# Optimization experiments

Measured on AMD Instinct MI355X. Metric: run time of the kernel, lower is better.

The kernel has to match this reference:

```python
import jax, jax.numpy as jnp
import numpy as np

NEG = 9000000000000000.0  # large negative multiplier from the original code

def setup_inputs() -> dict:
    key = jax.random.key(0)
    ks = jax.random.split(key, 7)
    B, N, DIN, H, DOUT = 128, 512, 256, 256, 256
    x = jax.random.normal(ks[0], (B, N, DIN), dtype=jnp.float32)
    # binary float mask (1 = attend, 0 = blocked), as used multiplicatively in the module
    mask = (jax.random.uniform(ks[1], (B, N, N)) > 0.5).astype(jnp.float32)
    def lin(k, fan_in, fan_out):
        kw, kb = jax.random.split(k)
        bound = 1.0 / np.sqrt(fan_in)
        W = jax.random.uniform(kw, (fan_in, fan_out), minval=-bound, maxval=bound, dtype=jnp.float32)
        b = jax.random.uniform(kb, (fan_out,), minval=-bound, maxval=bound, dtype=jnp.float32)
        return W, b
    Wv, bv = lin(ks[2], DIN, H)
    Wk, bk = lin(ks[3], DIN, H)
    Wq, bq = lin(ks[4], DIN, H)
    Wo, bo = lin(ks[5], H, DOUT)
    return {"x": x, "mask": mask, "Wv": Wv, "bv": bv, "Wk": Wk, "bk": bk,
            "Wq": Wq, "bq": bq, "Wo": Wo, "bo": bo}

def reference(x, mask, Wv, bv, Wk, bk, Wq, bq, Wo, bo):
    # x: [B,N,din], mask: [B,N,N]
    v = jax.nn.relu(jnp.einsum('bnd,dh->bnh', x, Wv) + bv)   # [B,N,H]
    q = jax.nn.relu(jnp.einsum('bnd,dh->bnh', x, Wq) + bq)   # [B,N,H]
    k = jax.nn.relu(jnp.einsum('bnd,dh->bnh', x, Wk) + bk)   # [B,N,H]
    scores = jnp.einsum('bnh,bmh->bnm', q, k)                 # [B,N,N]
    att = jax.nn.softmax(scores * mask - NEG * (1.0 - mask), axis=2)
    out = jnp.einsum('bnm,bmh->bnh', att, v)                  # [B,N,H]
    out = jax.nn.relu(jnp.einsum('bnh,ho->bno', out, Wo) + bo)
    return out
```

## Files before the change

kernel.cpp:

```cpp
#include <hip/hip_runtime.h>
#include <stdint.h>

typedef __attribute__((ext_vector_type(8))) __bf16 bf16x8;
typedef __attribute__((ext_vector_type(4))) float f32x4;
typedef __attribute__((ext_vector_type(8))) unsigned short ushort8;
typedef __attribute__((ext_vector_type(4))) unsigned short ushort4v;
typedef unsigned short u16;
typedef unsigned int u32;

__device__ __forceinline__ u16 f2bf(float f) {
    __bf16 h = (__bf16)f;
    return __builtin_bit_cast(u16, h);
}

__device__ __forceinline__ f32x4 mfma16(bf16x8 a, bf16x8 b, f32x4 c) {
    return __builtin_amdgcn_mfma_f32_16x16x32_bf16(a, b, c, 0, 0, 0);
}

typedef __attribute__((address_space(1))) const char g_char;
typedef __attribute__((address_space(3))) char l_char;
__device__ __forceinline__ void gload_lds16(const void* g, void* l) {
    __builtin_amdgcn_global_load_lds((g_char*)g, (l_char*)l, 16, 0, 0);
}

__global__ __launch_bounds__(256) void prep_w(
    const float* __restrict__ Wq, const float* __restrict__ Wk,
    const float* __restrict__ Wv, const float* __restrict__ Wo,
    u16* __restrict__ WT, u16* __restrict__ WOT)
{
    int idx = blockIdx.x * 256 + threadIdx.x;
    if (idx < 196608) {
        int j = idx >> 8, k = idx & 255;
        const float* W = (j < 256) ? Wq : (j < 512) ? Wk : Wv;
        WT[idx] = f2bf(W[k * 256 + (j & 255)]);
    } else {
        int t = idx - 196608;
        int j = t >> 8, k = t & 255;
        WOT[t] = f2bf(Wo[k * 256 + j]);
    }
}

__global__ __launch_bounds__(256, 2) void qkv_gemm(
    const float* __restrict__ X, const u16* __restrict__ WT,
    const float* __restrict__ bQ, const float* __restrict__ bK,
    const float* __restrict__ bV,
    u16* __restrict__ outQ, u16* __restrict__ outK, u16* __restrict__ outVT)
{
    __shared__ __align__(16) u16 As[128 * 256];
    __shared__ __align__(16) u16 Bs[128 * 64];
    const int tid = threadIdx.x;
    const int m0 = blockIdx.x * 128;

    #pragma unroll
    for (int i = 0; i < 32; ++i) {
        int flat = (i * 256 + tid) * 4;
        int r = flat >> 8, c = flat & 255;
        const f32x4 f = *reinterpret_cast<const f32x4*>(X + (size_t)(m0 + r) * 256 + c);
        ushort4v h;
        h.x = f2bf(f.x); h.y = f2bf(f.y); h.z = f2bf(f.z); h.w = f2bf(f.w);
        int byte = (r * 512 + c * 2) ^ ((r & 7) << 4);
        *reinterpret_cast<ushort4v*>(reinterpret_cast<char*>(As) + byte) = h;
    }

    const int lane = tid & 63, wid = tid >> 6;
    const int wr = wid >> 1, wc = wid & 1;
    const int lr = lane & 15, lg = lane >> 4;

    for (int cb = 0; cb < 6; ++cb) {
        const int jbase = cb * 128;
        f32x4 acc[4][4];
        #pragma unroll
        for (int a = 0; a < 4; ++a)
            #pragma unroll
            for (int b = 0; b < 4; ++b) acc[a][b] = (f32x4){0.f, 0.f, 0.f, 0.f};

        for (int kk = 0; kk < 256; kk += 64) {
            __syncthreads();
            #pragma unroll
            for (int i = 0; i < 4; ++i) {
                int e = (i * 256 + tid) * 8;
                int r = e >> 6, c = e & 63;
                ushort8 d = *reinterpret_cast<const ushort8*>(WT + (size_t)(jbase + r) * 256 + kk + c);
                int byte = (r * 128 + c * 2) ^ ((r & 7) << 4);
                *reinterpret_cast<ushort8*>(reinterpret_cast<char*>(Bs) + byte) = d;
            }
            __syncthreads();
            #pragma unroll
            for (int ks = 0; ks < 2; ++ks) {
                bf16x8 af[4], bfr[4];
                #pragma unroll
                for (int mt = 0; mt < 4; ++mt) {
                    int r = wr * 64 + mt * 16 + lr;
                    int byte = (r * 512 + (kk + ks * 32 + lg * 8) * 2) ^ ((r & 7) << 4);
                    af[mt] = *reinterpret_cast<const bf16x8*>(reinterpret_cast<const char*>(As) + byte);
                }
                #pragma unroll
                for (int nt = 0; nt < 4; ++nt) {
                    int r = wc * 64 + nt * 16 + lr;
                    int byte = (r * 128 + (ks * 32 + lg * 8) * 2) ^ ((r & 7) << 4);
                    bfr[nt] = *reinterpret_cast<const bf16x8*>(reinterpret_cast<const char*>(Bs) + byte);
                }
                #pragma unroll
                for (int mt = 0; mt < 4; ++mt)
                    #pragma unroll
                    for (int nt = 0; nt < 4; ++nt)
                        acc[mt][nt] = mfma16(af[mt], bfr[nt], acc[mt][nt]);
            }
        }
        const float* bias = (cb < 2) ? bQ : (cb < 4) ? bK : bV;
        float bcol[4];
        #pragma unroll
        for (int nt = 0; nt < 4; ++nt)
            bcol[nt] = bias[(jbase + wc * 64 + nt * 16 + lr) & 255];
        #pragma unroll
        for (int mt = 0; mt < 4; ++mt) {
            #pragma unroll
            for (int nt = 0; nt < 4; ++nt) {
                #pragma unroll
                for (int j = 0; j < 4; ++j) {
                    float v = fmaxf(acc[mt][nt][j] + bcol[nt], 0.f);
                    u16 h = f2bf(v);
                    int row = m0 + wr * 64 + mt * 16 + lg * 4 + j;
                    int col = jbase + wc * 64 + nt * 16 + lr;
                    if (cb < 2) {
                        outQ[(size_t)row * 256 + col] = h;
                    } else if (cb < 4) {
                        outK[(size_t)row * 256 + (col - 256)] = h;
                    } else {
                        int bb = row >> 9, n = row & 511;
                        outVT[(size_t)bb * 131072 + (size_t)(col - 512) * 512 + n] = h;
                    }
                }
            }
        }
    }
}

__global__ __launch_bounds__(512) void attn_kernel(
    const u16* __restrict__ Q, const u16* __restrict__ K,
    const u16* __restrict__ VT, const float* __restrict__ Mask,
    u16* __restrict__ Out)
{
    __shared__ __align__(16) u16 k_lds[2][32 * 256];
    __shared__ __align__(16) u16 v_lds[2][256 * 32];
    __shared__ __align__(16) u16 p_lds[8][16 * 32];
    const int tid = threadIdx.x;
    const int b  = blockIdx.x & 127;
    const int rb = blockIdx.x >> 7;
    const int lane = tid & 63, wid = tid >> 6;
    const int lr = lane & 15, lg = lane >> 4;
    const int n0 = rb * 128 + wid * 16;
    const u16* qbat = Q  + (size_t)b * 131072;
    const u16* kbat = K  + (size_t)b * 131072;
    const u16* vbat = VT + (size_t)b * 131072;
    const float* mrow = Mask + ((size_t)b * 512 + n0 + lg * 4) * 512;

    auto stage = [&](int buf, int kt) {
        #pragma unroll
        for (int i = 0; i < 2; ++i) {
            int p = (i * 512 + tid) * 16;
            int krow = p >> 9, kcol2 = p & 511;
            int scol2 = kcol2 ^ ((krow & 7) << 4);
            const char* gk = reinterpret_cast<const char*>(kbat + (size_t)(kt * 32 + krow) * 256) + scol2;
            char* lk = reinterpret_cast<char*>(k_lds[buf]) + i * 8192 + wid * 1024;
            gload_lds16(gk, lk);
            int vrow = p >> 6, vcol2 = p & 63;
            const char* gv = reinterpret_cast<const char*>(vbat + (size_t)vrow * 512 + kt * 32) + vcol2;
            char* lv = reinterpret_cast<char*>(v_lds[buf]) + i * 8192 + wid * 1024;
            gload_lds16(gv, lv);
        }
    };

    bf16x8 qf[8];
    #pragma unroll
    for (int ks = 0; ks < 8; ++ks)
        qf[ks] = *reinterpret_cast<const bf16x8*>(
            qbat + (size_t)(n0 + lr) * 256 + ks * 32 + lg * 8);

    stage(0, 0);
    float mf[2][4];
    #pragma unroll
    for (int ct = 0; ct < 2; ++ct)
        #pragma unroll
        for (int j = 0; j < 4; ++j)
            mf[ct][j] = __builtin_nontemporal_load(mrow + (size_t)j * 512 + ct * 16 + lr);

    f32x4 acc[16];
    #pragma unroll
    for (int i = 0; i < 16; ++i) acc[i] = (f32x4){0.f, 0.f, 0.f, 0.f};
    float mreg[4], lreg[4];
    #pragma unroll
    for (int j = 0; j < 4; ++j) { mreg[j] = -__builtin_inff(); lreg[j] = 0.f; }

    __syncthreads();

    for (int kt = 0; kt < 16; ++kt) {
        const int cur = kt & 1;
        if (kt < 15) stage(cur ^ 1, kt + 1);

        u32 mb = 0;
        #pragma unroll
        for (int ct = 0; ct < 2; ++ct)
            #pragma unroll
            for (int j = 0; j < 4; ++j)
                mb |= (mf[ct][j] > 0.5f ? 1u : 0u) << (ct * 4 + j);
        if (kt < 15) {
            #pragma unroll
            for (int ct = 0; ct < 2; ++ct)
                #pragma unroll
                for (int j = 0; j < 4; ++j)
                    mf[ct][j] = __builtin_nontemporal_load(
                        mrow + (size_t)j * 512 + (kt + 1) * 32 + ct * 16 + lr);
        }

        f32x4 s[2];
        s[0] = (f32x4){0.f, 0.f, 0.f, 0.f};
        s[1] = (f32x4){0.f, 0.f, 0.f, 0.f};
        const char* kbase = reinterpret_cast<const char*>(k_lds[cur]);
        __builtin_amdgcn_s_setprio(1);
        #pragma unroll
        for (int ks = 0; ks < 8; ++ks) {
            #pragma unroll
            for (int ct = 0; ct < 2; ++ct) {
                int krow = ct * 16 + lr;
                int byte = (krow * 512 + (ks * 32 + lg * 8) * 2) ^ ((krow & 7) << 4);
                bf16x8 kf = *reinterpret_cast<const bf16x8*>(kbase + byte);
                s[ct] = mfma16(qf[ks], kf, s[ct]);
            }
        }
        __builtin_amdgcn_s_setprio(0);

        float p[2][4];
        #pragma unroll
        for (int ct = 0; ct < 2; ++ct)
            #pragma unroll
            for (int j = 0; j < 4; ++j)
                p[ct][j] = ((mb >> (ct * 4 + j)) & 1u) ? s[ct][j] : -9.0e15f;

        float r0j[4];
        bool need = false;
        #pragma unroll
        for (int j = 0; j < 4; ++j) {
            float r0 = fmaxf(p[0][j], p[1][j]);
            r0 = fmaxf(r0, __shfl_xor(r0, 1));
            r0 = fmaxf(r0, __shfl_xor(r0, 2));
            r0 = fmaxf(r0, __shfl_xor(r0, 4));
            r0 = fmaxf(r0, __shfl_xor(r0, 8));
            r0j[j] = r0;
            need = need || (r0 > mreg[j]);
        }
        if (__any(need)) {
            #pragma unroll
            for (int j = 0; j < 4; ++j) {
                float mnew = fmaxf(mreg[j], r0j[j]);
                float sc = __expf(mreg[j] - mnew);
                mreg[j] = mnew;
                lreg[j] *= sc;
                #pragma unroll
                for (int ht = 0; ht < 16; ++ht) acc[ht][j] *= sc;
            }
        }
        #pragma unroll
        for (int j = 0; j < 4; ++j) {
            float ps = 0.f;
            #pragma unroll
            for (int ct = 0; ct < 2; ++ct) {
                float e = __expf(p[ct][j] - mreg[j]);
                p[ct][j] = e;
                ps += e;
            }
            lreg[j] += ps;
        }

        #pragma unroll
        for (int ct = 0; ct < 2; ++ct)
            #pragma unroll
            for (int j = 0; j < 4; ++j) {
                int byte = (lg * 4 + j) * 64 + (ct * 16 + lr) * 2;
                *reinterpret_cast<u16*>(reinterpret_cast<char*>(p_lds[wid]) + byte) = f2bf(p[ct][j]);
            }

        bf16x8 pf = *reinterpret_cast<const bf16x8*>(
            reinterpret_cast<const char*>(p_lds[wid]) + lr * 64 + lg * 16);
        const char* vbase = reinterpret_cast<const char*>(v_lds[cur]);
        __builtin_amdgcn_s_setprio(1);
        #pragma unroll
        for (int ht = 0; ht < 16; ++ht) {
            bf16x8 vf = *reinterpret_cast<const bf16x8*>(vbase + (ht * 16 + lr) * 64 + lg * 16);
            acc[ht] = mfma16(pf, vf, acc[ht]);
        }
        __builtin_amdgcn_s_setprio(0);

        __syncthreads();
    }

    #pragma unroll
    for (int j = 0; j < 4; ++j) {
        float lt = lreg[j];
        lt += __shfl_xor(lt, 1);
        lt += __shfl_xor(lt, 2);
        lt += __shfl_xor(lt, 4);
        lt += __shfl_xor(lt, 8);
        float inv = 1.0f / lt;
        int qn = n0 + lg * 4 + j;
        u16* orow = Out + ((size_t)b * 512 + qn) * 256;
        #pragma unroll
        for (int ht = 0; ht < 16; ++ht)
            orow[ht * 16 + lr] = f2bf(acc[ht][j] * inv);
    }
}

__global__ __launch_bounds__(256, 2) void out_gemm(
    const u16* __restrict__ A, const u16* __restrict__ WOT,
    const float* __restrict__ bO, float* __restrict__ Out)
{
    __shared__ __align__(16) u16 As[128 * 256];
    __shared__ __align__(16) u16 Bs[128 * 64];
    const int tid = threadIdx.x;
    const int m0 = blockIdx.x * 128;

    #pragma unroll
    for (int i = 0; i < 16; ++i) {
        int e = (i * 256 + tid) * 8;
        int r = e >> 8, c = e & 255;
        ushort8 d = *reinterpret_cast<const ushort8*>(A + (size_t)(m0 + r) * 256 + c);
        int byte = (r * 512 + c * 2) ^ ((r & 7) << 4);
        *reinterpret_cast<ushort8*>(reinterpret_cast<char*>(As) + byte) = d;
    }

    const int lane = tid & 63, wid = tid >> 6;
    const int wr = wid >> 1, wc = wid & 1;
    const int lr = lane & 15, lg = lane >> 4;

    for (int cb = 0; cb < 2; ++cb) {
        const int jbase = cb * 128;
        f32x4 acc[4][4];
        #pragma unroll
        for (int a = 0; a < 4; ++a)
            #pragma unroll
            for (int b = 0; b < 4; ++b) acc[a][b] = (f32x4){0.f, 0.f, 0.f, 0.f};

        for (int kk = 0; kk < 256; kk += 64) {
            __syncthreads();
            #pragma unroll
            for (int i = 0; i < 4; ++i) {
                int e = (i * 256 + tid) * 8;
                int r = e >> 6, c = e & 63;
                ushort8 d = *reinterpret_cast<const ushort8*>(WOT + (size_t)(jbase + r) * 256 + kk + c);
                int byte = (r * 128 + c * 2) ^ ((r & 7) << 4);
                *reinterpret_cast<ushort8*>(reinterpret_cast<char*>(Bs) + byte) = d;
            }
            __syncthreads();
            #pragma unroll
            for (int ks = 0; ks < 2; ++ks) {
                bf16x8 af[4], bfr[4];
                #pragma unroll
                for (int mt = 0; mt < 4; ++mt) {
                    int r = wr * 64 + mt * 16 + lr;
                    int byte = (r * 512 + (kk + ks * 32 + lg * 8) * 2) ^ ((r & 7) << 4);
                    af[mt] = *reinterpret_cast<const bf16x8*>(reinterpret_cast<const char*>(As) + byte);
                }
                #pragma unroll
                for (int nt = 0; nt < 4; ++nt) {
                    int r = wc * 64 + nt * 16 + lr;
                    int byte = (r * 128 + (ks * 32 + lg * 8) * 2) ^ ((r & 7) << 4);
                    bfr[nt] = *reinterpret_cast<const bf16x8*>(reinterpret_cast<const char*>(Bs) + byte);
                }
                #pragma unroll
                for (int mt = 0; mt < 4; ++mt)
                    #pragma unroll
                    for (int nt = 0; nt < 4; ++nt)
                        acc[mt][nt] = mfma16(af[mt], bfr[nt], acc[mt][nt]);
            }
        }
        float bcol[4];
        #pragma unroll
        for (int nt = 0; nt < 4; ++nt)
            bcol[nt] = bO[jbase + wc * 64 + nt * 16 + lr];
        #pragma unroll
        for (int mt = 0; mt < 4; ++mt) {
            #pragma unroll
            for (int nt = 0; nt < 4; ++nt) {
                #pragma unroll
                for (int j = 0; j < 4; ++j) {
                    float v = fmaxf(acc[mt][nt][j] + bcol[nt], 0.f);
                    int row = m0 + wr * 64 + mt * 16 + lg * 4 + j;
                    int col = jbase + wc * 64 + nt * 16 + lr;
                    Out[(size_t)row * 256 + col] = v;
                }
            }
        }
    }
}

extern "C" void kernel_launch(void* const* d_in, const int* in_sizes, int n_in,
                              void* d_out, int out_size, void* d_ws, size_t ws_size,
                              hipStream_t stream) {
    const float* x    = (const float*)d_in[0];
    const float* mask = (const float*)d_in[1];
    const float* Wv   = (const float*)d_in[2];
    const float* bv   = (const float*)d_in[3];
    const float* Wk   = (const float*)d_in[4];
    const float* bk   = (const float*)d_in[5];
    const float* Wq   = (const float*)d_in[6];
    const float* bq   = (const float*)d_in[7];
    const float* Wo   = (const float*)d_in[8];
    const float* bo   = (const float*)d_in[9];
    float* out = (float*)d_out;

    char* ws = (char*)d_ws;
    u16* WT  = (u16*)(ws);
    u16* WOT = (u16*)(ws + 393216);
    u16* Qb  = (u16*)(ws + 524288);
    u16* Kb  = (u16*)(ws + 524288 + 33554432);
    u16* VTb = (u16*)(ws + 524288 + 2 * 33554432);

    prep_w<<<1024, 256, 0, stream>>>(Wq, Wk, Wv, Wo, WT, WOT);
    qkv_gemm<<<512, 256, 0, stream>>>(x, WT, bq, bk, bv, Qb, Kb, VTb);
    attn_kernel<<<512, 512, 0, stream>>>(Qb, Kb, VTb, mask, Qb);
    out_gemm<<<512, 256, 0, stream>>>(Qb, WOT, bo, out);
}
```

Baseline: 196.5 us.

## Fuse output projection GEMM into attention kernel epilogue

The attention kernel now stages its normalized per-wave output tile in LDS and immediately multiplies it by the transposed output weights, applying bias and ReLU and writing fp32 results. This removes the separate out_gemm launch and the bf16 intermediate write/read of the attention output. In exchange every wave streams the full output weight matrix from global memory/L2 without LDS sharing, which raises cache traffic and register pressure in the epilogue.

Result: slower. 227.6 us (+15.8%).

```diff
diff --git a/kernel.cpp b/kernel.cpp
--- a/kernel.cpp
+++ b/kernel.cpp
@@ -139,11 +139,13 @@
 __global__ __launch_bounds__(512) void attn_kernel(
     const u16* __restrict__ Q, const u16* __restrict__ K,
     const u16* __restrict__ VT, const float* __restrict__ Mask,
-    u16* __restrict__ Out)
+    const u16* __restrict__ WOT, const float* __restrict__ bO,
+    float* __restrict__ Out)
 {
-    __shared__ __align__(16) u16 k_lds[2][32 * 256];
-    __shared__ __align__(16) u16 v_lds[2][256 * 32];
-    __shared__ __align__(16) u16 p_lds[8][16 * 32];
+    __shared__ __align__(16) char smem[73728];
+    u16* k_lds = reinterpret_cast<u16*>(smem);
+    u16* v_lds = reinterpret_cast<u16*>(smem + 32768);
+    u16* p_lds = reinterpret_cast<u16*>(smem + 65536);
     const int tid = threadIdx.x;
     const int b  = blockIdx.x & 127;
     const int rb = blockIdx.x >> 7;
@@ -162,11 +164,11 @@
             int krow = p >> 9, kcol2 = p & 511;
             int scol2 = kcol2 ^ ((krow & 7) << 4);
             const char* gk = reinterpret_cast<const char*>(kbat + (size_t)(kt * 32 + krow) * 256) + scol2;
-            char* lk = reinterpret_cast<char*>(k_lds[buf]) + i * 8192 + wid * 1024;
+            char* lk = reinterpret_cast<char*>(k_lds) + buf * 16384 + i * 8192 + wid * 1024;
             gload_lds16(gk, lk);
             int vrow = p >> 6, vcol2 = p & 63;
             const char* gv = reinterpret_cast<const char*>(vbat + (size_t)vrow * 512 + kt * 32) + vcol2;
-            char* lv = reinterpret_cast<char*>(v_lds[buf]) + i * 8192 + wid * 1024;
+            char* lv = reinterpret_cast<char*>(v_lds) + buf * 16384 + i * 8192 + wid * 1024;
             gload_lds16(gv, lv);
         }
     };
@@ -216,7 +218,7 @@
         f32x4 s[2];
         s[0] = (f32x4){0.f, 0.f, 0.f, 0.f};
         s[1] = (f32x4){0.f, 0.f, 0.f, 0.f};
-        const char* kbase = reinterpret_cast<const char*>(k_lds[cur]);
+        const char* kbase = reinterpret_cast<const char*>(k_lds) + cur * 16384;
         __builtin_amdgcn_s_setprio(1);
         #pragma unroll
         for (int ks = 0; ks < 8; ++ks) {
@@ -277,12 +279,12 @@
             #pragma unroll
             for (int j = 0; j < 4; ++j) {
                 int byte = (lg * 4 + j) * 64 + (ct * 16 + lr) * 2;
-                *reinterpret_cast<u16*>(reinterpret_cast<char*>(p_lds[wid]) + byte) = f2bf(p[ct][j]);
+                *reinterpret_cast<u16*>(reinterpret_cast<char*>(p_lds) + wid * 1024 + byte) = f2bf(p[ct][j]);
             }
 
         bf16x8 pf = *reinterpret_cast<const bf16x8*>(
-            reinterpret_cast<const char*>(p_lds[wid]) + lr * 64 + lg * 16);
-        const char* vbase = reinterpret_cast<const char*>(v_lds[cur]);
+            reinterpret_cast<const char*>(p_lds) + wid * 1024 + lr * 64 + lg * 16);
+        const char* vbase = reinterpret_cast<const char*>(v_lds) + cur * 16384;
         __builtin_amdgcn_s_setprio(1);
         #pragma unroll
         for (int ht = 0; ht < 16; ++ht) {
@@ -294,6 +296,7 @@
         __syncthreads();
     }
 
+    char* ao = smem + wid * 8192;
     #pragma unroll
     for (int j = 0; j < 4; ++j) {
         float lt = lreg[j];
@@ -302,93 +305,39 @@
         lt += __shfl_xor(lt, 4);
         lt += __shfl_xor(lt, 8);
         float inv = 1.0f / lt;
-        int qn = n0 + lg * 4 + j;
-        u16* orow = Out + ((size_t)b * 512 + qn) * 256;
-        #pragma unroll
-        for (int ht = 0; ht < 16; ++ht)
-            orow[ht * 16 + lr] = f2bf(acc[ht][j] * inv);
-    }
-}
-
-__global__ __launch_bounds__(256, 2) void out_gemm(
-    const u16* __restrict__ A, const u16* __restrict__ WOT,
-    const float* __restrict__ bO, float* __restrict__ Out)
-{
-    __shared__ __align__(16) u16 As[128 * 256];
-    __shared__ __align__(16) u16 Bs[128 * 64];
-    const int tid = threadIdx.x;
-    const int m0 = blockIdx.x * 128;
-
-    #pragma unroll
-    for (int i = 0; i < 16; ++i) {
-        int e = (i * 256 + tid) * 8;
-        int r = e >> 8, c = e & 255;
-        ushort8 d = *reinterpret_cast<const ushort8*>(A + (size_t)(m0 + r) * 256 + c);
-        int byte = (r * 512 + c * 2) ^ ((r & 7) << 4);
-        *reinterpret_cast<ushort8*>(reinterpret_cast<char*>(As) + byte) = d;
-    }
-
-    const int lane = tid & 63, wid = tid >> 6;
-    const int wr = wid >> 1, wc = wid & 1;
-    const int lr = lane & 15, lg = lane >> 4;
-
-    for (int cb = 0; cb < 2; ++cb) {
-        const int jbase = cb * 128;
-        f32x4 acc[4][4];
-        #pragma unroll
-        for (int a = 0; a < 4; ++a)
-            #pragma unroll
-            for (int b = 0; b < 4; ++b) acc[a][b] = (f32x4){0.f, 0.f, 0.f, 0.f};
-
-        for (int kk = 0; kk < 256; kk += 64) {
-            __syncthreads();
-            #pragma unroll
-            for (int i = 0; i < 4; ++i) {
-                int e = (i * 256 + tid) * 8;
-                int r = e >> 6, c = e & 63;
-                ushort8 d = *reinterpret_cast<const ushort8*>(WOT + (size_t)(jbase + r) * 256 + kk + c);
-                int byte = (r * 128 + c * 2) ^ ((r & 7) << 4);
-                *reinterpret_cast<ushort8*>(reinterpret_cast<char*>(Bs) + byte) = d;
-            }
-            __syncthreads();
-            #pragma unroll
-            for (int ks = 0; ks < 2; ++ks) {
-                bf16x8 af[4], bfr[4];
-                #pragma unroll
-                for (int mt = 0; mt < 4; ++mt) {
-                    int r = wr * 64 + mt * 16 + lr;
-                    int byte = (r * 512 + (kk + ks * 32 + lg * 8) * 2) ^ ((r & 7) << 4);
-                    af[mt] = *reinterpret_cast<const bf16x8*>(reinterpret_cast<const char*>(As) + byte);
-                }
-                #pragma unroll
-                for (int nt = 0; nt < 4; ++nt) {
-                    int r = wc * 64 + nt * 16 + lr;
-                    int byte = (r * 128 + (ks * 32 + lg * 8) * 2) ^ ((r & 7) << 4);
-                    bfr[nt] = *reinterpret_cast<const bf16x8*>(reinterpret_cast<const char*>(Bs) + byte);
-                }
-                #pragma unroll
-                for (int mt = 0; mt < 4; ++mt)
-                    #pragma unroll
-                    for (int nt = 0; nt < 4; ++nt)
-                        acc[mt][nt] = mfma16(af[mt], bfr[nt], acc[mt][nt]);
-            }
-        }
-        float bcol[4];
-        #pragma unroll
-        for (int nt = 0; nt < 4; ++nt)
-            bcol[nt] = bO[jbase + wc * 64 + nt * 16 + lr];
-        #pragma unroll
-        for (int mt = 0; mt < 4; ++mt) {
-            #pragma unroll
-            for (int nt = 0; nt < 4; ++nt) {
-                #pragma unroll
-                for (int j = 0; j < 4; ++j) {
-                    float v = fmaxf(acc[mt][nt][j] + bcol[nt], 0.f);
-                    int row = m0 + wr * 64 + mt * 16 + lg * 4 + j;
-                    int col = jbase + wc * 64 + nt * 16 + lr;
-                    Out[(size_t)row * 256 + col] = v;
-                }
-            }
+        int row = lg * 4 + j;
+        #pragma unroll
+        for (int ht = 0; ht < 16; ++ht) {
+            int byte = (row * 512 + (ht * 16 + lr) * 2) ^ ((row & 7) << 4);
+            *reinterpret_cast<u16*>(ao + byte) = f2bf(acc[ht][j] * inv);
+        }
+    }
+
+    f32x4 oacc[16];
+    #pragma unroll
+    for (int i = 0; i < 16; ++i) oacc[i] = (f32x4){0.f, 0.f, 0.f, 0.f};
+    #pragma unroll
+    for (int ks = 0; ks < 8; ++ks) {
+        int abyte = (lr * 512 + (ks * 32 + lg * 8) * 2) ^ ((lr & 7) << 4);
+        bf16x8 af = *reinterpret_cast<const bf16x8*>(ao + abyte);
+        __builtin_amdgcn_s_setprio(1);
+        #pragma unroll
+        for (int ct = 0; ct < 16; ++ct) {
+            bf16x8 bf = *reinterpret_cast<const bf16x8*>(
+                WOT + (size_t)(ct * 16 + lr) * 256 + ks * 32 + lg * 8);
+            oacc[ct] = mfma16(af, bf, oacc[ct]);
+        }
+        __builtin_amdgcn_s_setprio(0);
+    }
+
+    float* orow = Out + ((size_t)b * 512 + n0 + lg * 4) * 256;
+    #pragma unroll
+    for (int ct = 0; ct < 16; ++ct) {
+        float bc = bO[ct * 16 + lr];
+        #pragma unroll
+        for (int j = 0; j < 4; ++j) {
+            float v = fmaxf(oacc[ct][j] + bc, 0.f);
+            orow[(size_t)j * 256 + ct * 16 + lr] = v;
         }
     }
 }
@@ -417,6 +366,5 @@
 
     prep_w<<<1024, 256, 0, stream>>>(Wq, Wk, Wv, Wo, WT, WOT);
     qkv_gemm<<<512, 256, 0, stream>>>(x, WT, bq, bk, bv, Qb, Kb, VTb);
-    attn_kernel<<<512, 512, 0, stream>>>(Qb, Kb, VTb, mask, Qb);
-    out_gemm<<<512, 256, 0, stream>>>(Qb, WOT, bo, out);
-}
+    attn_kernel<<<512, 512, 0, stream>>>(Qb, Kb, VTb, mask, WOT, bo, out);
+}
```

## Transpose MFMA operands so each lane owns one query row in attention

Applied to the files above, without the earlier changes.

The MFMA operands are swapped so the score and output accumulators are transposed, and each lane now holds four key columns of a single query row. This turns row-max and row-sum reductions into in-register ops plus two cross-group shuffles, and allows vectorized 16-byte mask loads and 8-byte output stores. It also adds an XOR swizzle to the V tile in LDS and pads the P buffer rows to cut bank conflicts. The risk is correctness, since the swizzle and index changes must match across staging, reads and writes.

New measurement: 187.5 us. 1.05x faster.

```diff
diff --git a/kernel.cpp b/kernel.cpp
--- a/kernel.cpp
+++ b/kernel.cpp
@@ -143,7 +143,7 @@
 {
     __shared__ __align__(16) u16 k_lds[2][32 * 256];
     __shared__ __align__(16) u16 v_lds[2][256 * 32];
-    __shared__ __align__(16) u16 p_lds[8][16 * 32];
+    __shared__ __align__(16) char p_lds[8 * 1280];
     const int tid = threadIdx.x;
     const int b  = blockIdx.x & 127;
     const int rb = blockIdx.x >> 7;
@@ -153,7 +153,8 @@
     const u16* qbat = Q  + (size_t)b * 131072;
     const u16* kbat = K  + (size_t)b * 131072;
     const u16* vbat = VT + (size_t)b * 131072;
-    const float* mrow = Mask + ((size_t)b * 512 + n0 + lg * 4) * 512;
+    const float* mbase = Mask + ((size_t)b * 512 + n0 + lr) * 512;
+    char* pw = p_lds + wid * 1280;
 
     auto stage = [&](int buf, int kt) {
         #pragma unroll
@@ -164,8 +165,10 @@
             const char* gk = reinterpret_cast<const char*>(kbat + (size_t)(kt * 32 + krow) * 256) + scol2;
             char* lk = reinterpret_cast<char*>(k_lds[buf]) + i * 8192 + wid * 1024;
             gload_lds16(gk, lk);
-            int vrow = p >> 6, vcol2 = p & 63;
-            const char* gv = reinterpret_cast<const char*>(vbat + (size_t)vrow * 512 + kt * 32) + vcol2;
+            int vrow = p >> 6;
+            int chunk = (p >> 4) & 3;
+            int schunk = chunk ^ (vrow & 3);
+            const char* gv = reinterpret_cast<const char*>(vbat + (size_t)vrow * 512 + kt * 32) + schunk * 16;
             char* lv = reinterpret_cast<char*>(v_lds[buf]) + i * 8192 + wid * 1024;
             gload_lds16(gv, lv);
         }
@@ -178,19 +181,16 @@
             qbat + (size_t)(n0 + lr) * 256 + ks * 32 + lg * 8);
 
     stage(0, 0);
-    float mf[2][4];
+    f32x4 mf[2];
     #pragma unroll
     for (int ct = 0; ct < 2; ++ct)
-        #pragma unroll
-        for (int j = 0; j < 4; ++j)
-            mf[ct][j] = __builtin_nontemporal_load(mrow + (size_t)j * 512 + ct * 16 + lr);
+        mf[ct] = __builtin_nontemporal_load(
+            reinterpret_cast<const f32x4*>(mbase + ct * 16 + lg * 4));
 
     f32x4 acc[16];
     #pragma unroll
     for (int i = 0; i < 16; ++i) acc[i] = (f32x4){0.f, 0.f, 0.f, 0.f};
-    float mreg[4], lreg[4];
-    #pragma unroll
-    for (int j = 0; j < 4; ++j) { mreg[j] = -__builtin_inff(); lreg[j] = 0.f; }
+    float mreg = -__builtin_inff(), lreg = 0.f;
 
     __syncthreads();
 
@@ -207,10 +207,8 @@
         if (kt < 15) {
             #pragma unroll
             for (int ct = 0; ct < 2; ++ct)
-                #pragma unroll
-                for (int j = 0; j < 4; ++j)
-                    mf[ct][j] = __builtin_nontemporal_load(
-                        mrow + (size_t)j * 512 + (kt + 1) * 32 + ct * 16 + lr);
+                mf[ct] = __builtin_nontemporal_load(reinterpret_cast<const f32x4*>(
+                    mbase + (kt + 1) * 32 + ct * 16 + lg * 4));
         }
 
         f32x4 s[2];
@@ -225,7 +223,7 @@
                 int krow = ct * 16 + lr;
                 int byte = (krow * 512 + (ks * 32 + lg * 8) * 2) ^ ((krow & 7) << 4);
                 bf16x8 kf = *reinterpret_cast<const bf16x8*>(kbase + byte);
-                s[ct] = mfma16(qf[ks], kf, s[ct]);
+                s[ct] = mfma16(kf, qf[ks], s[ct]);
             }
         }
         __builtin_amdgcn_s_setprio(0);
@@ -237,76 +235,69 @@
             for (int j = 0; j < 4; ++j)
                 p[ct][j] = ((mb >> (ct * 4 + j)) & 1u) ? s[ct][j] : -9.0e15f;
 
-        float r0j[4];
-        bool need = false;
-        #pragma unroll
-        for (int j = 0; j < 4; ++j) {
-            float r0 = fmaxf(p[0][j], p[1][j]);
-            r0 = fmaxf(r0, __shfl_xor(r0, 1));
-            r0 = fmaxf(r0, __shfl_xor(r0, 2));
-            r0 = fmaxf(r0, __shfl_xor(r0, 4));
-            r0 = fmaxf(r0, __shfl_xor(r0, 8));
-            r0j[j] = r0;
-            need = need || (r0 > mreg[j]);
-        }
+        float r0 = p[0][0];
+        r0 = fmaxf(r0, p[0][1]); r0 = fmaxf(r0, p[0][2]); r0 = fmaxf(r0, p[0][3]);
+        r0 = fmaxf(r0, p[1][0]); r0 = fmaxf(r0, p[1][1]);
+        r0 = fmaxf(r0, p[1][2]); r0 = fmaxf(r0, p[1][3]);
+        r0 = fmaxf(r0, __shfl_xor(r0, 16));
+        r0 = fmaxf(r0, __shfl_xor(r0, 32));
+        bool need = (r0 > mreg);
         if (__any(need)) {
+            float mnew = fmaxf(mreg, r0);
+            float sc = __expf(mreg - mnew);
+            mreg = mnew;
+            lreg *= sc;
+            #pragma unroll
+            for (int ht = 0; ht < 16; ++ht) {
+                acc[ht][0] *= sc; acc[ht][1] *= sc;
+                acc[ht][2] *= sc; acc[ht][3] *= sc;
+            }
+        }
+        float ps = 0.f;
+        #pragma unroll
+        for (int ct = 0; ct < 2; ++ct)
             #pragma unroll
             for (int j = 0; j < 4; ++j) {
-                float mnew = fmaxf(mreg[j], r0j[j]);
-                float sc = __expf(mreg[j] - mnew);
-                mreg[j] = mnew;
-                lreg[j] *= sc;
-                #pragma unroll
-                for (int ht = 0; ht < 16; ++ht) acc[ht][j] *= sc;
-            }
-        }
-        #pragma unroll
-        for (int j = 0; j < 4; ++j) {
-            float ps = 0.f;
-            #pragma unroll
-            for (int ct = 0; ct < 2; ++ct) {
-                float e = __expf(p[ct][j] - mreg[j]);
+                float e = __expf(p[ct][j] - mreg);
                 p[ct][j] = e;
                 ps += e;
             }
-            lreg[j] += ps;
-        }
-
-        #pragma unroll
-        for (int ct = 0; ct < 2; ++ct)
-            #pragma unroll
-            for (int j = 0; j < 4; ++j) {
-                int byte = (lg * 4 + j) * 64 + (ct * 16 + lr) * 2;
-                *reinterpret_cast<u16*>(reinterpret_cast<char*>(p_lds[wid]) + byte) = f2bf(p[ct][j]);
-            }
-
-        bf16x8 pf = *reinterpret_cast<const bf16x8*>(
-            reinterpret_cast<const char*>(p_lds[wid]) + lr * 64 + lg * 16);
+        lreg += ps;
+
+        #pragma unroll
+        for (int ct = 0; ct < 2; ++ct) {
+            ushort4v w;
+            w.x = f2bf(p[ct][0]); w.y = f2bf(p[ct][1]);
+            w.z = f2bf(p[ct][2]); w.w = f2bf(p[ct][3]);
+            *reinterpret_cast<ushort4v*>(pw + lr * 80 + ct * 32 + lg * 8) = w;
+        }
+
+        bf16x8 pf = *reinterpret_cast<const bf16x8*>(pw + lr * 80 + lg * 16);
         const char* vbase = reinterpret_cast<const char*>(v_lds[cur]);
         __builtin_amdgcn_s_setprio(1);
         #pragma unroll
         for (int ht = 0; ht < 16; ++ht) {
-            bf16x8 vf = *reinterpret_cast<const bf16x8*>(vbase + (ht * 16 + lr) * 64 + lg * 16);
-            acc[ht] = mfma16(pf, vf, acc[ht]);
+            int hrow = ht * 16 + lr;
+            int byte = (hrow * 64 + lg * 16) ^ ((hrow & 3) << 4);
+            bf16x8 vf = *reinterpret_cast<const bf16x8*>(vbase + byte);
+            acc[ht] = mfma16(vf, pf, acc[ht]);
         }
         __builtin_amdgcn_s_setprio(0);
 
         __syncthreads();
     }
 
-    #pragma unroll
-    for (int j = 0; j < 4; ++j) {
-        float lt = lreg[j];
-        lt += __shfl_xor(lt, 1);
-        lt += __shfl_xor(lt, 2);
-        lt += __shfl_xor(lt, 4);
-        lt += __shfl_xor(lt, 8);
-        float inv = 1.0f / lt;
-        int qn = n0 + lg * 4 + j;
-        u16* orow = Out + ((size_t)b * 512 + qn) * 256;
-        #pragma unroll
-        for (int ht = 0; ht < 16; ++ht)
-            orow[ht * 16 + lr] = f2bf(acc[ht][j] * inv);
+    float lt = lreg;
+    lt += __shfl_xor(lt, 16);
+    lt += __shfl_xor(lt, 32);
+    float inv = 1.0f / lt;
+    u16* orow = Out + ((size_t)b * 512 + n0 + lr) * 256;
+    #pragma unroll
+    for (int ht = 0; ht < 16; ++ht) {
+        ushort4v w;
+        w.x = f2bf(acc[ht][0] * inv); w.y = f2bf(acc[ht][1] * inv);
+        w.z = f2bf(acc[ht][2] * inv); w.w = f2bf(acc[ht][3] * inv);
+        *reinterpret_cast<ushort4v*>(orow + ht * 16 + lg * 4) = w;
     }
 }
 
```
